# Optimization experiments

Hardware: AMD Instinct MI355X
Metric: run time of the kernel (lower is better)

## Reference

```python
import jax, jax.numpy as jnp
import numpy as np

N_NODES = 100000
N_EDGES = 1600000
D_IN = 64
D_HID = 64
N_CLS = 4


def setup_inputs() -> dict:
    key = jax.random.key(0)
    ks = jax.random.split(key, 8)
    s = lambda d: 1.0 / np.sqrt(d)
    return {
        "node_features": jax.random.normal(ks[0], (N_NODES, D_IN), jnp.float32),
        "edge_src": jax.random.randint(ks[1], (N_EDGES,), 0, N_NODES, jnp.int32),
        "edge_dst": jax.random.randint(ks[2], (N_EDGES,), 0, N_NODES, jnp.int32),
        "W_self1": jax.random.normal(ks[3], (D_IN, D_HID), jnp.float32) * s(D_IN),
        "b_self1": jnp.zeros((D_HID,), jnp.float32),
        "W_neigh1": jax.random.normal(ks[4], (D_IN, D_HID), jnp.float32) * s(D_IN),
        "W_self2": jax.random.normal(ks[5], (D_HID, N_CLS), jnp.float32) * s(D_HID),
        "b_self2": jnp.zeros((N_CLS,), jnp.float32),
        "W_neigh2": jax.random.normal(ks[6], (D_HID, N_CLS), jnp.float32) * s(D_HID),
    }


def _sage_mean(h, edge_src, edge_dst, W_self, b_self, W_neigh, n_nodes):
    # mean aggregation over in-neighbors: gather src feats, segment-sum by dst
    msg_sum = jax.ops.segment_sum(h[edge_src], edge_dst, num_segments=n_nodes)
    deg = jax.ops.segment_sum(
        jnp.ones_like(edge_dst, dtype=h.dtype), edge_dst, num_segments=n_nodes
    )
    h_neigh = msg_sum / jnp.maximum(deg, 1.0)[:, None]
    # DGL SAGEConv: fc_self (with bias) + fc_neigh (no bias)
    return h @ W_self + b_self + h_neigh @ W_neigh


def reference(node_features, edge_src, edge_dst, W_self1, b_self1, W_neigh1,
              W_self2, b_self2, W_neigh2):
    n = node_features.shape[0]
    h1 = jnp.tanh(_sage_mean(node_features, edge_src, edge_dst,
                             W_self1, b_self1, W_neigh1, n))
    logits = _sage_mean(h1, edge_src, edge_dst, W_self2, b_self2, W_neigh2, n)
    return logits
```

## Files before the change

### kernel.cpp

```cpp
#include <hip/hip_runtime.h>
#include <hip/hip_bf16.h>
#include <stdint.h>

typedef unsigned char  u8;
typedef unsigned short u16;
typedef unsigned int   u32;
typedef __attribute__((ext_vector_type(8))) short bf16x8;
typedef __attribute__((ext_vector_type(2))) float f32x2;
typedef __attribute__((ext_vector_type(4))) float f32x4;
typedef __attribute__((ext_vector_type(4))) int   i32x4;
typedef __attribute__((ext_vector_type(2))) u32   u32x2;
typedef __attribute__((ext_vector_type(4))) u32   u32x4;

#define BKT_SHIFT 8
#define BKT_NODES 256
#define CAP 5120
#define BINBLK 512
#define GEMMBLK 512

__device__ __forceinline__ float bf2f(u16 u) { return __uint_as_float(((u32)u) << 16); }
__device__ __forceinline__ u16 f2bf(float f) {
    u32 u = __float_as_uint(f);
    u += 0x7FFFu + ((u >> 16) & 1u);
    return (u16)(u >> 16);
}
__device__ __forceinline__ int pkbf(float a, float b) {
    return (int)__builtin_amdgcn_perm(__float_as_uint(b), __float_as_uint(a), 0x07060302u);
}
__device__ __forceinline__ u8 f2fp8(float v) {
    int p = __builtin_amdgcn_cvt_pk_fp8_f32(v, v, 0, false);
    return (u8)(p & 0xff);
}


__global__ __launch_bounds__(256) void k_front(const float* __restrict__ X,
                                               const float* __restrict__ Ws,
                                               const float* __restrict__ b1,
                                               const float* __restrict__ Wn,
                                               u16* __restrict__ Zb,
                                               u8* __restrict__ Y,
                                               int n,
                                               const int* __restrict__ src,
                                               const int* __restrict__ dst,
                                               int* __restrict__ offT,
                                               u32* __restrict__ binned,
                                               int E, int chunk, int nb) {
    __shared__ __align__(16) char sm[31744];
    int t = threadIdx.x;

    if ((int)blockIdx.x < BINBLK) {
        u32* keys = (u32*)sm;
        int* h    = (int*)(sm + 12800);
        int* cur  = (int*)(sm + 14400);
        int* ws4  = (int*)(sm + 16000);
        int blk = blockIdx.x;
        int beg = blk * chunk, end = min(beg + chunk, E), m = max(0, end - beg);

        for (int i = t; i < nb; i += 256) h[i] = 0;
        __syncthreads();
        for (int i = beg + t; i < end; i += 256) atomicAdd(&h[dst[i] >> BKT_SHIFT], 1);
        __syncthreads();
        int lane = t & 63, w = t >> 6;
        int e0 = 2 * t, e1 = 2 * t + 1;
        int h0 = (e0 < nb) ? h[e0] : 0;
        int h1 = (e1 < nb) ? h[e1] : 0;
        int s = h0 + h1;
        int incl = s;
#pragma unroll
        for (int o = 1; o < 64; o <<= 1) {
            int x = __shfl_up(incl, o, 64);
            if (lane >= o) incl += x;
        }
        if (lane == 63) ws4[w] = incl;
        __syncthreads();
        if (t == 0) {
            int run = 0;
#pragma unroll
            for (int i = 0; i < 4; i++) { ws4[4 + i] = run; run += ws4[i]; }
        }
        __syncthreads();
        int excl = incl - s + ws4[4 + w];
        int* orow = offT + (size_t)blk * (nb + 1);
        if (e0 < nb) { cur[e0] = excl;      orow[e0] = excl; }
        if (e1 < nb) { cur[e1] = excl + h0; orow[e1] = excl + h0; }
        if (t == 255) orow[nb] = excl + s;
        __syncthreads();
        for (int i = beg + t; i < end; i += 256) {
            int d = dst[i], bk = d >> BKT_SHIFT;
            int p = atomicAdd(&cur[bk], 1);
            keys[p] = ((u32)src[i] << BKT_SHIFT) | (u32)(d & (BKT_NODES - 1));
        }
        __syncthreads();
        u32* outp = binned + (size_t)blk * chunk;
        for (int i = t; i < m; i += 256) outp[i] = keys[i];
        return;
    }

    u16* wl = (u16*)sm;
    for (int i = t; i < 8192; i += 256) {
        int k = i >> 7, c = i & 127;
        float wv = (c < 64) ? Ws[k * 64 + c] : Wn[k * 64 + (c - 64)];
        wl[k * 132 + c] = f2bf(wv);
    }
    __syncthreads();

    int wid = t >> 6, lane = t & 63;
    int lrow = lane & 15, lquad = lane >> 4;

    bf16x8 bfrag[8][2];
#pragma unroll
    for (int ct = 0; ct < 8; ct++)
#pragma unroll
        for (int kf = 0; kf < 2; kf++)
#pragma unroll
            for (int j = 0; j < 8; j++)
                bfrag[ct][kf][j] = (short)wl[(kf * 32 + lquad * 8 + j) * 132 + ct * 16 + lrow];

    float bias[4];
#pragma unroll
    for (int ct = 0; ct < 4; ct++) bias[ct] = b1[ct * 16 + lrow];

    u16* Zs = (u16*)(sm + 16896 + wid * 3712);
    u8*  Ys = (u8*)(sm + 16896 + wid * 3712 + 2432);
    int srow = lane >> 2, sseg = lane & 3;

    int tiles = n >> 4;
    int tstride = GEMMBLK * 4;
    for (int tile = (blockIdx.x - BINBLK) * 4 + wid; tile < tiles; tile += tstride) {
        int nb4 = tile << 4;

        const float* xp = X + (size_t)(nb4 + lrow) * 64 + lquad * 8;
        f32x4 x0 = *(const f32x4*)(xp);
        f32x4 x1 = *(const f32x4*)(xp + 4);
        f32x4 x2 = *(const f32x4*)(xp + 32);
        f32x4 x3 = *(const f32x4*)(xp + 36);
        i32x4 p0, p1;
        p0.x = pkbf(x0.x, x0.y); p0.y = pkbf(x0.z, x0.w);
        p0.z = pkbf(x1.x, x1.y); p0.w = pkbf(x1.z, x1.w);
        p1.x = pkbf(x2.x, x2.y); p1.y = pkbf(x2.z, x2.w);
        p1.z = pkbf(x3.x, x3.y); p1.w = pkbf(x3.z, x3.w);
        bf16x8 af0 = __builtin_bit_cast(bf16x8, p0);
        bf16x8 af1 = __builtin_bit_cast(bf16x8, p1);

        f32x4 acc[8];
#pragma unroll
        for (int ct = 0; ct < 8; ct++) {
            f32x4 c = {0.f, 0.f, 0.f, 0.f};
            c = __builtin_amdgcn_mfma_f32_16x16x32_bf16(af0, bfrag[ct][0], c, 0, 0, 0);
            c = __builtin_amdgcn_mfma_f32_16x16x32_bf16(af1, bfrag[ct][1], c, 0, 0, 0);
            acc[ct] = c;
        }

#pragma unroll
        for (int ct = 0; ct < 4; ct++)
#pragma unroll
            for (int r = 0; r < 4; r++)
                Zs[(lquad * 4 + r) * 76 + ct * 16 + lrow] = f2bf(acc[ct][r] + bias[ct]);
#pragma unroll
        for (int ct = 0; ct < 4; ct++)
#pragma unroll
            for (int r = 0; r < 4; r++)
                Ys[(lquad * 4 + r) * 80 + ct * 16 + lrow] = f2fp8(acc[ct + 4][r]);

        u32x4 z0 = *(const u32x4*)&Zs[srow * 76 + sseg * 16];
        u32x4 z1 = *(const u32x4*)&Zs[srow * 76 + sseg * 16 + 8];
        u32x4 yv = *(const u32x4*)&Ys[srow * 80 + sseg * 16];
        *(u32x4*)(Zb + (size_t)(nb4 + srow) * 64 + sseg * 16) = z0;
        *(u32x4*)(Zb + (size_t)(nb4 + srow) * 64 + sseg * 16 + 8) = z1;
        *(u32x4*)(Y + (size_t)(nb4 + srow) * 64 + sseg * 16) = yv;
    }
}


__global__ __launch_bounds__(512) void k_csrg1(const u32* __restrict__ binned,
                                               const int* __restrict__ offT,
                                               const u16* __restrict__ Zb,
                                               const u8* __restrict__ Y,
                                               const float* __restrict__ Ws2,
                                               const float* __restrict__ b2,
                                               const float* __restrict__ Wn2,
                                               int* __restrict__ rpb,
                                               int* __restrict__ rpe,
                                               int* __restrict__ col,
                                               float* __restrict__ P,
                                               u16* __restrict__ Q,
                                               int chunk, int nb, int n) {
    __shared__ __align__(16) u32 ed[CAP];
    __shared__ __align__(16) u32 srt[CAP];
    __shared__ int gst[BINBLK], gln[BINBLK], soff[BINBLK];
    __shared__ int cnt[BKT_NODES];
    __shared__ float wl[64 * 9];
    __shared__ int wsum[8], woff[8];
    __shared__ int stot;
    int b = blockIdx.x, t = threadIdx.x;
    int lane = t & 63, w = t >> 6;

    {
        int k = t >> 3, c = t & 7;
        float v = (c < 4) ? Ws2[k * 4 + c] : Wn2[k * 4 + (c - 4)];
        wl[((k & 7) * 8 + (k >> 3)) * 9 + c] = v;
    }
    {
        const int* row = offT + (size_t)t * (nb + 1);
        int s = row[b], e = row[b + 1];
        gst[t] = t * chunk + s;
        gln[t] = e - s;
    }
    float bb0 = b2[0], bb1 = b2[1], bb2 = b2[2], bb3 = b2[3];
    __syncthreads();

    int v = gln[t];
    int incl = v;
#pragma unroll
    for (int o = 1; o < 64; o <<= 1) {
        int x = __shfl_up(incl, o, 64);
        if (lane >= o) incl += x;
    }
    if (lane == 63) wsum[w] = incl;
    __syncthreads();
    if (t == 0) {
        int run = 0;
#pragma unroll
        for (int i = 0; i < 8; i++) { woff[i] = run; run += wsum[i]; }
        stot = run;
    }
    __syncthreads();
    soff[t] = incl - v + woff[w];
    __syncthreads();
    int total = min(stot, CAP);

    {
        int sg = lane >> 3, sl = lane & 7;
        for (int k0 = w * 8 + sg; k0 < BINBLK; k0 += 64) {
            int g = gst[k0], L = gln[k0], o = soff[k0];
            for (int i = sl; i < L; i += 8)
                if (o + i < CAP) ed[o + i] = binned[g + i];
        }
    }
    if (t < BKT_NODES) cnt[t] = 0;
    __syncthreads();

    for (int i = t; i < total; i += 512)
        atomicAdd(&cnt[ed[i] & (BKT_NODES - 1)], 1);
    __syncthreads();

    int v2 = (t < BKT_NODES) ? cnt[t] : 0;
    int incl2 = v2;
#pragma unroll
    for (int o = 1; o < 64; o <<= 1) {
        int x = __shfl_up(incl2, o, 64);
        if (lane >= o) incl2 += x;
    }
    if (lane == 63) wsum[w] = incl2;
    __syncthreads();
    if (t == 0) {
        int run = 0;
#pragma unroll
        for (int i = 0; i < 8; i++) { woff[i] = run; run += wsum[i]; }
    }
    __syncthreads();
    int excl2 = incl2 - v2 + woff[w];
    int cb = b * CAP;
    if (t < BKT_NODES) {
        int gnode = b * BKT_NODES + t;
        if (gnode < n) { rpb[gnode] = cb + excl2; rpe[gnode] = cb + excl2 + v2; }
        gst[t] = excl2;
        gln[t] = v2;
        cnt[t] = excl2;
    }
    __syncthreads();

    for (int i = t; i < total; i += 512) {
        u32 e = ed[i];
        int p = atomicAdd(&cnt[e & (BKT_NODES - 1)], 1);
        srt[p] = e >> BKT_SHIFT;
    }
    __syncthreads();

    for (int i = t; i < total; i += 512) col[cb + i] = (int)srt[i];

    int gid = t >> 3, l8 = t & 7;
    const u8* yb = Y + (size_t)l8 * 8;
#pragma unroll 1
    for (int r = 0; r < 4; r++) {
        int ln_ = gid + r * 64;
        int node = b * BKT_NODES + ln_;
        if (node >= n) continue;
        int s0 = gst[ln_], L = gln[ln_];
        float a[8];
#pragma unroll
        for (int j = 0; j < 8; j++) a[j] = 0.f;
        int e = 0;
        for (; e + 8 <= L; e += 8) {
            int s_[8];
#pragma unroll
            for (int j = 0; j < 8; j++) s_[j] = (int)srt[s0 + e + j];
            u32x2 y_[8];
#pragma unroll
            for (int j = 0; j < 8; j++) y_[j] = *(const u32x2*)(yb + (size_t)s_[j] * 64);
#pragma unroll
            for (int j = 0; j < 8; j++) {
                f32x2 lo0 = __builtin_amdgcn_cvt_pk_f32_fp8(y_[j].x, false);
                f32x2 hi0 = __builtin_amdgcn_cvt_pk_f32_fp8(y_[j].x, true);
                f32x2 lo1 = __builtin_amdgcn_cvt_pk_f32_fp8(y_[j].y, false);
                f32x2 hi1 = __builtin_amdgcn_cvt_pk_f32_fp8(y_[j].y, true);
                a[0] += lo0.x; a[1] += lo0.y; a[2] += hi0.x; a[3] += hi0.y;
                a[4] += lo1.x; a[5] += lo1.y; a[6] += hi1.x; a[7] += hi1.y;
            }
        }
        for (; e < L; e++) {
            int sj = (int)srt[s0 + e];
            u32x2 yw = *(const u32x2*)(yb + (size_t)sj * 64);
            f32x2 lo0 = __builtin_amdgcn_cvt_pk_f32_fp8(yw.x, false);
            f32x2 hi0 = __builtin_amdgcn_cvt_pk_f32_fp8(yw.x, true);
            f32x2 lo1 = __builtin_amdgcn_cvt_pk_f32_fp8(yw.y, false);
            f32x2 hi1 = __builtin_amdgcn_cvt_pk_f32_fp8(yw.y, true);
            a[0] += lo0.x; a[1] += lo0.y; a[2] += hi0.x; a[3] += hi0.y;
            a[4] += lo1.x; a[5] += lo1.y; a[6] += hi1.x; a[7] += hi1.y;
        }

        float deg = (float)L;
        float inv = (deg > 0.f) ? 1.f / deg : 0.f;
        u32x4 zr = *(const u32x4*)(Zb + (size_t)node * 64 + l8 * 8);
        float h[8];
#pragma unroll
        for (int j = 0; j < 8; j++) {
            u32 word = (j < 2) ? zr.x : (j < 4) ? zr.y : (j < 6) ? zr.z : zr.w;
            u16 zv = (j & 1) ? (u16)(word >> 16) : (u16)(word & 0xffff);
            h[j] = tanhf(bf2f(zv) + a[j] * inv);
        }

        float rr[8];
#pragma unroll
        for (int c = 0; c < 8; c++) rr[c] = 0.f;
#pragma unroll
        for (int j = 0; j < 8; j++) {
            float hj = h[j];
            const float* wp = &wl[(j * 8 + l8) * 9];
#pragma unroll
            for (int c = 0; c < 8; c++) rr[c] += hj * wp[c];
        }
#pragma unroll
        for (int m = 1; m < 8; m <<= 1)
#pragma unroll
            for (int c = 0; c < 8; c++) rr[c] += __shfl_xor(rr[c], m, 64);

        if (l8 == 0) {
            *(float4*)(P + (size_t)node * 4) =
                make_float4(rr[0] + bb0, rr[1] + bb1, rr[2] + bb2, rr[3] + bb3);
            ushort4 qv;
            qv.x = f2bf(rr[4]); qv.y = f2bf(rr[5]); qv.z = f2bf(rr[6]); qv.w = f2bf(rr[7]);
            *(ushort4*)(Q + (size_t)node * 4) = qv;
        }
    }
}


__global__ __launch_bounds__(256) void k_gather2(const int* __restrict__ rpb,
                                                 const int* __restrict__ rpe,
                                                 const int* __restrict__ col,
                                                 const float* __restrict__ P,
                                                 const u16* __restrict__ Q,
                                                 float* __restrict__ out, int n) {
    int t = threadIdx.x;
    int g = t >> 4, l = t & 15;
    int node = blockIdx.x * 16 + g;
    if (node >= n) return;
    int beg = rpb[node], end = rpe[node];
    float a0 = 0.f, a1 = 0.f, a2 = 0.f, a3 = 0.f;
    for (int e = beg + l; e < end; e += 16) {
        ushort4 qv = *(const ushort4*)(Q + (size_t)col[e] * 4);
        a0 += bf2f(qv.x); a1 += bf2f(qv.y); a2 += bf2f(qv.z); a3 += bf2f(qv.w);
    }
#pragma unroll
    for (int m = 1; m < 16; m <<= 1) {
        a0 += __shfl_xor(a0, m, 64);
        a1 += __shfl_xor(a1, m, 64);
        a2 += __shfl_xor(a2, m, 64);
        a3 += __shfl_xor(a3, m, 64);
    }
    if (l == 0) {
        float deg = (float)(end - beg);
        float inv = (deg > 0.f) ? 1.f / deg : 0.f;
        float4 p = *(const float4*)(P + (size_t)node * 4);
        *(float4*)(out + (size_t)node * 4) =
            make_float4(p.x + a0 * inv, p.y + a1 * inv,
                        p.z + a2 * inv, p.w + a3 * inv);
    }
}


extern "C" void kernel_launch(void* const* d_in, const int* in_sizes, int n_in,
                              void* d_out, int out_size, void* d_ws, size_t ws_size,
                              hipStream_t stream) {
    const float* X   = (const float*)d_in[0];
    const int* esrc  = (const int*)d_in[1];
    const int* edst  = (const int*)d_in[2];
    const float* Ws1 = (const float*)d_in[3];
    const float* b1  = (const float*)d_in[4];
    const float* Wn1 = (const float*)d_in[5];
    const float* Ws2 = (const float*)d_in[6];
    const float* b2  = (const float*)d_in[7];
    const float* Wn2 = (const float*)d_in[8];
    float* out = (float*)d_out;

    const int n = in_sizes[0] / 64;
    const int E = in_sizes[1];
    const int nb = (n + BKT_NODES - 1) >> BKT_SHIFT;
    const int chunk = (E + BINBLK - 1) / BINBLK;

    size_t off = 0;
    char* base = (char*)d_ws;
    auto give = [&](size_t bytes) -> char* {
        char* p = base + off;
        off += (bytes + 255) & ~(size_t)255;
        return p;
    };
    int*   offT   = (int*)give((size_t)BINBLK * (nb + 1) * 4);
    int*   rpb    = (int*)give((size_t)n * 4);
    int*   rpe    = (int*)give((size_t)n * 4);
    u32*   binned = (u32*)give((size_t)BINBLK * chunk * 4);
    int*   col    = (int*)give((size_t)nb * CAP * 4);
    u16*   Zb     = (u16*)give((size_t)n * 64 * 2);
    u8*    Y      = (u8*)give((size_t)n * 64);
    float* P      = (float*)give((size_t)n * 4 * 4);
    u16*   Q      = (u16*)give((size_t)n * 4 * 2);

    k_front<<<BINBLK + GEMMBLK, 256, 0, stream>>>(
        X, Ws1, b1, Wn1, Zb, Y, n,
        esrc, edst, offT, binned, E, chunk, nb);

    k_csrg1<<<nb, 512, 0, stream>>>(binned, offT, Zb, Y, Ws2, b2, Wn2,
                                    rpb, rpe, col, P, Q, chunk, nb, n);

    k_gather2<<<(n + 15) / 16, 256, 0, stream>>>(rpb, rpe, col, P, Q, out, n);
}
```

Before: 157.3 us.

## Cache edge src/dst in registers and transpose bucket offset table layout

The binning blocks now load each thread's dst/src edges once into a fixed-size register array (MAXPT=13 per thread). Both the histogram pass and the scatter pass read from these registers, so dst and src are no longer fetched from global memory twice. The per-block bucket offset table is also transposed to bucket-major, so each CSR block reads its 512 per-bin offsets with coalesced loads instead of strided ones. The register array assumes chunk <= 13*256 edges per block, which silently drops edges for larger inputs and adds register pressure.

```diff
diff --git a/kernel.cpp b/kernel.cpp
--- a/kernel.cpp
+++ b/kernel.cpp
@@ -17,6 +17,7 @@
 #define CAP 5120
 #define BINBLK 512
 #define GEMMBLK 512
+#define MAXPT 13
 
 __device__ __forceinline__ float bf2f(u16 u) { return __uint_as_float(((u32)u) << 16); }
 __device__ __forceinline__ u16 f2bf(float f) {
@@ -56,9 +57,20 @@
         int blk = blockIdx.x;
         int beg = blk * chunk, end = min(beg + chunk, E), m = max(0, end - beg);
 
+        int rs_[MAXPT], rd_[MAXPT];
+#pragma unroll
+        for (int j = 0; j < MAXPT; j++) {
+            int i = beg + t + j * 256;
+            bool ok = i < end;
+            rd_[j] = ok ? dst[i] : -1;
+            rs_[j] = ok ? src[i] : 0;
+        }
+
         for (int i = t; i < nb; i += 256) h[i] = 0;
         __syncthreads();
-        for (int i = beg + t; i < end; i += 256) atomicAdd(&h[dst[i] >> BKT_SHIFT], 1);
+#pragma unroll
+        for (int j = 0; j < MAXPT; j++)
+            if (rd_[j] >= 0) atomicAdd(&h[rd_[j] >> BKT_SHIFT], 1);
         __syncthreads();
         int lane = t & 63, w = t >> 6;
         int e0 = 2 * t, e1 = 2 * t + 1;
@@ -80,15 +92,17 @@
         }
         __syncthreads();
         int excl = incl - s + ws4[4 + w];
-        int* orow = offT + (size_t)blk * (nb + 1);
-        if (e0 < nb) { cur[e0] = excl;      orow[e0] = excl; }
-        if (e1 < nb) { cur[e1] = excl + h0; orow[e1] = excl + h0; }
-        if (t == 255) orow[nb] = excl + s;
-        __syncthreads();
-        for (int i = beg + t; i < end; i += 256) {
-            int d = dst[i], bk = d >> BKT_SHIFT;
-            int p = atomicAdd(&cur[bk], 1);
-            keys[p] = ((u32)src[i] << BKT_SHIFT) | (u32)(d & (BKT_NODES - 1));
+        if (e0 < nb) { cur[e0] = excl;      offT[(size_t)e0 * BINBLK + blk] = excl; }
+        if (e1 < nb) { cur[e1] = excl + h0; offT[(size_t)e1 * BINBLK + blk] = excl + h0; }
+        if (t == 255) offT[(size_t)nb * BINBLK + blk] = excl + s;
+        __syncthreads();
+#pragma unroll
+        for (int j = 0; j < MAXPT; j++) {
+            if (rd_[j] >= 0) {
+                int d = rd_[j], bk = d >> BKT_SHIFT;
+                int p = atomicAdd(&cur[bk], 1);
+                keys[p] = ((u32)rs_[j] << BKT_SHIFT) | (u32)(d & (BKT_NODES - 1));
+            }
         }
         __syncthreads();
         u32* outp = binned + (size_t)blk * chunk;
@@ -201,8 +215,8 @@
         wl[((k & 7) * 8 + (k >> 3)) * 9 + c] = v;
     }
     {
-        const int* row = offT + (size_t)t * (nb + 1);
-        int s = row[b], e = row[b + 1];
+        int s = offT[(size_t)b * BINBLK + t];
+        int e = offT[(size_t)(b + 1) * BINBLK + t];
         gst[t] = t * chunk + s;
         gln[t] = e - s;
     }
@@ -416,7 +430,7 @@
         off += (bytes + 255) & ~(size_t)255;
         return p;
     };
-    int*   offT   = (int*)give((size_t)BINBLK * (nb + 1) * 4);
+    int*   offT   = (int*)give((size_t)(nb + 1) * BINBLK * 4);
     int*   rpb    = (int*)give((size_t)n * 4);
     int*   rpe    = (int*)give((size_t)n * 4);
     u32*   binned = (u32*)give((size_t)BINBLK * chunk * 4);
```

After: 159.7 us. Within noise of the previous version (+1.6%).

## Scatter binned edges directly into per-bucket slabs via global atomic fill counters

Applied to the files above, without the earlier changes.

The binning blocks now reserve space in a per-bucket global slab with one atomicAdd per bucket and write their edge keys straight into contiguous bucket slabs. The offset table and per-block binned layout go away. The CSR kernel then does a single contiguous load per bucket instead of a prefix scan over 512 source-block segments followed by scattered segment reads. This adds a memset launch and global atomics, and makes slab placement order nondeterministic, though that order is re-sorted later.

```diff
diff --git a/kernel.cpp b/kernel.cpp
--- a/kernel.cpp
+++ b/kernel.cpp
@@ -42,17 +42,19 @@
                                                int n,
                                                const int* __restrict__ src,
                                                const int* __restrict__ dst,
-                                               int* __restrict__ offT,
-                                               u32* __restrict__ binned,
+                                               u32* __restrict__ slab,
+                                               int* __restrict__ bfill,
                                                int E, int chunk, int nb) {
     __shared__ __align__(16) char sm[31744];
     int t = threadIdx.x;
 
     if ((int)blockIdx.x < BINBLK) {
         u32* keys = (u32*)sm;
-        int* h    = (int*)(sm + 12800);
-        int* cur  = (int*)(sm + 14400);
-        int* ws4  = (int*)(sm + 16000);
+        u16* bb16 = (u16*)(sm + 12800);
+        int* h    = (int*)(sm + 19200);
+        int* cur  = (int*)(sm + 20800);
+        int* sbase= (int*)(sm + 22400);
+        int* ws4  = (int*)(sm + 24000);
         int blk = blockIdx.x;
         int beg = blk * chunk, end = min(beg + chunk, E), m = max(0, end - beg);
 
@@ -80,19 +82,27 @@
         }
         __syncthreads();
         int excl = incl - s + ws4[4 + w];
-        int* orow = offT + (size_t)blk * (nb + 1);
-        if (e0 < nb) { cur[e0] = excl;      orow[e0] = excl; }
-        if (e1 < nb) { cur[e1] = excl + h0; orow[e1] = excl + h0; }
-        if (t == 255) orow[nb] = excl + s;
+        if (e0 < nb) cur[e0] = excl;
+        if (e1 < nb) cur[e1] = excl + h0;
         __syncthreads();
         for (int i = beg + t; i < end; i += 256) {
             int d = dst[i], bk = d >> BKT_SHIFT;
             int p = atomicAdd(&cur[bk], 1);
             keys[p] = ((u32)src[i] << BKT_SHIFT) | (u32)(d & (BKT_NODES - 1));
-        }
-        __syncthreads();
-        u32* outp = binned + (size_t)blk * chunk;
-        for (int i = t; i < m; i += 256) outp[i] = keys[i];
+            bb16[p] = (u16)bk;
+        }
+        __syncthreads();
+        for (int bk = t; bk < nb; bk += 256) {
+            int len = h[bk];
+            sbase[bk] = (len > 0) ? atomicAdd(&bfill[bk], len) : 0;
+        }
+        __syncthreads();
+        for (int i = t; i < m; i += 256) {
+            int bk = (int)bb16[i];
+            int seg_start = cur[bk] - h[bk];
+            int o = sbase[bk] + (i - seg_start);
+            if (o < CAP) slab[(size_t)bk * CAP + o] = keys[i];
+        }
         return;
     }
 
@@ -172,8 +182,8 @@
 }
 
 
-__global__ __launch_bounds__(512) void k_csrg1(const u32* __restrict__ binned,
-                                               const int* __restrict__ offT,
+__global__ __launch_bounds__(512) void k_csrg1(const u32* __restrict__ slab,
+                                               const int* __restrict__ bfill,
                                                const u16* __restrict__ Zb,
                                                const u8* __restrict__ Y,
                                                const float* __restrict__ Ws2,
@@ -184,14 +194,12 @@
                                                int* __restrict__ col,
                                                float* __restrict__ P,
                                                u16* __restrict__ Q,
-                                               int chunk, int nb, int n) {
+                                               int nb, int n) {
     __shared__ __align__(16) u32 ed[CAP];
     __shared__ __align__(16) u32 srt[CAP];
-    __shared__ int gst[BINBLK], gln[BINBLK], soff[BINBLK];
-    __shared__ int cnt[BKT_NODES];
+    __shared__ int nst[BKT_NODES], ndeg[BKT_NODES], cnt[BKT_NODES];
     __shared__ float wl[64 * 9];
     __shared__ int wsum[8], woff[8];
-    __shared__ int stot;
     int b = blockIdx.x, t = threadIdx.x;
     int lane = t & 63, w = t >> 6;
 
@@ -200,43 +208,10 @@
         float v = (c < 4) ? Ws2[k * 4 + c] : Wn2[k * 4 + (c - 4)];
         wl[((k & 7) * 8 + (k >> 3)) * 9 + c] = v;
     }
-    {
-        const int* row = offT + (size_t)t * (nb + 1);
-        int s = row[b], e = row[b + 1];
-        gst[t] = t * chunk + s;
-        gln[t] = e - s;
-    }
     float bb0 = b2[0], bb1 = b2[1], bb2 = b2[2], bb3 = b2[3];
-    __syncthreads();
-
-    int v = gln[t];
-    int incl = v;
-#pragma unroll
-    for (int o = 1; o < 64; o <<= 1) {
-        int x = __shfl_up(incl, o, 64);
-        if (lane >= o) incl += x;
-    }
-    if (lane == 63) wsum[w] = incl;
-    __syncthreads();
-    if (t == 0) {
-        int run = 0;
-#pragma unroll
-        for (int i = 0; i < 8; i++) { woff[i] = run; run += wsum[i]; }
-        stot = run;
-    }
-    __syncthreads();
-    soff[t] = incl - v + woff[w];
-    __syncthreads();
-    int total = min(stot, CAP);
-
-    {
-        int sg = lane >> 3, sl = lane & 7;
-        for (int k0 = w * 8 + sg; k0 < BINBLK; k0 += 64) {
-            int g = gst[k0], L = gln[k0], o = soff[k0];
-            for (int i = sl; i < L; i += 8)
-                if (o + i < CAP) ed[o + i] = binned[g + i];
-        }
-    }
+    int total = min(bfill[b], CAP);
+    const u32* sp = slab + (size_t)b * CAP;
+    for (int i = t; i < total; i += 512) ed[i] = sp[i];
     if (t < BKT_NODES) cnt[t] = 0;
     __syncthreads();
 
@@ -264,8 +239,8 @@
     if (t < BKT_NODES) {
         int gnode = b * BKT_NODES + t;
         if (gnode < n) { rpb[gnode] = cb + excl2; rpe[gnode] = cb + excl2 + v2; }
-        gst[t] = excl2;
-        gln[t] = v2;
+        nst[t] = excl2;
+        ndeg[t] = v2;
         cnt[t] = excl2;
     }
     __syncthreads();
@@ -286,7 +261,7 @@
         int ln_ = gid + r * 64;
         int node = b * BKT_NODES + ln_;
         if (node >= n) continue;
-        int s0 = gst[ln_], L = gln[ln_];
+        int s0 = nst[ln_], L = ndeg[ln_];
         float a[8];
 #pragma unroll
         for (int j = 0; j < 8; j++) a[j] = 0.f;
@@ -416,22 +391,24 @@
         off += (bytes + 255) & ~(size_t)255;
         return p;
     };
-    int*   offT   = (int*)give((size_t)BINBLK * (nb + 1) * 4);
+    int*   bfill  = (int*)give((size_t)nb * 4);
     int*   rpb    = (int*)give((size_t)n * 4);
     int*   rpe    = (int*)give((size_t)n * 4);
-    u32*   binned = (u32*)give((size_t)BINBLK * chunk * 4);
+    u32*   slab   = (u32*)give((size_t)nb * CAP * 4);
     int*   col    = (int*)give((size_t)nb * CAP * 4);
     u16*   Zb     = (u16*)give((size_t)n * 64 * 2);
     u8*    Y      = (u8*)give((size_t)n * 64);
     float* P      = (float*)give((size_t)n * 4 * 4);
     u16*   Q      = (u16*)give((size_t)n * 4 * 2);
 
+    hipMemsetAsync(bfill, 0, (size_t)nb * 4, stream);
+
     k_front<<<BINBLK + GEMMBLK, 256, 0, stream>>>(
         X, Ws1, b1, Wn1, Zb, Y, n,
-        esrc, edst, offT, binned, E, chunk, nb);
-
-    k_csrg1<<<nb, 512, 0, stream>>>(binned, offT, Zb, Y, Ws2, b2, Wn2,
-                                    rpb, rpe, col, P, Q, chunk, nb, n);
+        esrc, edst, slab, bfill, E, chunk, nb);
+
+    k_csrg1<<<nb, 512, 0, stream>>>(slab, bfill, Zb, Y, Ws2, b2, Wn2,
+                                    rpb, rpe, col, P, Q, nb, n);
 
     k_gather2<<<(n + 15) / 16, 256, 0, stream>>>(rpb, rpe, col, P, Q, out, n);
 }
```

Measured after the change: 165.1 us. 5.0% more time.
